# Kernel tuning notes

Measured on AMD Instinct MI355X. Metric: run time of the kernel, lower is better.

The kernel has to match this reference:

```python
import jax, jax.numpy as jnp
import numpy as np

C = 1024
D = C // 8  # query/key channel dim


def setup_inputs() -> dict:
    key = jax.random.key(0)
    ks = jax.random.split(key, 8)
    x = jax.random.normal(ks[0], (8, C, 2048), dtype=jnp.float32)
    # 1x1 Conv1d == per-position linear over channels: weight [out, in], bias [out]
    s_qk = 1.0 / np.sqrt(C)
    Wq = jax.random.uniform(ks[1], (D, C), jnp.float32, -s_qk, s_qk)
    bq = jax.random.uniform(ks[2], (D,), jnp.float32, -s_qk, s_qk)
    Wk = jax.random.uniform(ks[3], (D, C), jnp.float32, -s_qk, s_qk)
    bk = jax.random.uniform(ks[4], (D,), jnp.float32, -s_qk, s_qk)
    Wv = jax.random.uniform(ks[5], (C, C), jnp.float32, -s_qk, s_qk)
    bv = jax.random.uniform(ks[6], (C,), jnp.float32, -s_qk, s_qk)
    gamma = jnp.zeros((1,), dtype=jnp.float32)
    return {"x": x, "Wq": Wq, "bq": bq, "Wk": Wk, "bk": bk, "Wv": Wv, "bv": bv, "gamma": gamma}


def reference(x, Wq, bq, Wk, bk, Wv, bv, gamma):
    # x: [b, c, l]
    q = jnp.einsum('dc,bcl->bdl', Wq, x) + bq[None, :, None]  # [b, d, l]
    k = jnp.einsum('dc,bcl->bdl', Wk, x) + bk[None, :, None]  # [b, d, l]
    v = jnp.einsum('oc,bcl->bol', Wv, x) + bv[None, :, None]  # [b, c, l]
    energy = jnp.einsum('bdi,bdj->bij', q, k)                  # [b, l, l] (no scale, as in source)
    attention = jax.nn.softmax(energy, axis=-1)
    out = jnp.einsum('bcj,bij->bci', v, attention)             # value @ attention^T
    return gamma * out + x
```

## Files before the change

kernel.cpp:

```cpp
#include <hip/hip_runtime.h>
#include <hip/hip_bf16.h>
#include <stdint.h>

#define B_ 8
#define C_ 1024
#define D_ 128
#define L_ 2048

typedef __attribute__((ext_vector_type(8))) short short8;
typedef __attribute__((ext_vector_type(4))) float floatx4;

#define GLDS16(g, l)                                                          \
    __builtin_amdgcn_global_load_lds(                                         \
        (const __attribute__((address_space(1))) uint32_t*)(g),               \
        (__attribute__((address_space(3))) uint32_t*)(l), 16, 0, 0)

__device__ inline float b2f(uint16_t u) {
    union { uint32_t i; float f; } x; x.i = (uint32_t)u << 16; return x.f;
}
__device__ inline uint16_t f2b(float f) {
    union { uint32_t i; float f; } x; x.f = f;
    uint32_t r = (x.i + 0x7fff + ((x.i >> 16) & 1)) >> 16;
    return (uint16_t)r;
}

__global__ void cast_f32_bf16(const float* __restrict__ src, uint16_t* __restrict__ dst, int n) {
    int i = blockIdx.x * 256 + threadIdx.x;
    if (i < n) dst[i] = f2b(src[i]);
}

__global__ __launch_bounds__(256) void transpose_cast(const float* __restrict__ x, uint16_t* __restrict__ xT) {
    __shared__ float tile[32][33];
    int b = blockIdx.z;
    int l0 = blockIdx.x * 32, c0 = blockIdx.y * 32;
    int tx = threadIdx.x, ty = threadIdx.y;
    const float* xb = x + (size_t)b * C_ * L_;
#pragma unroll
    for (int i = 0; i < 4; i++)
        tile[ty + i * 8][tx] = xb[(size_t)(c0 + ty + i * 8) * L_ + l0 + tx];
    __syncthreads();
    uint16_t* xtb = xT + (size_t)b * L_ * C_;
#pragma unroll
    for (int i = 0; i < 4; i++) {
        int l = l0 + ty + i * 8, c = c0 + tx;
        xtb[(size_t)l * C_ + c] = f2b(tile[tx][ty + i * 8]);
    }
}

template <int EPI>
__global__ __launch_bounds__(256) void gemm_nt(
    const uint16_t* __restrict__ A, const uint16_t* __restrict__ B,
    long sA, long sB, const float* __restrict__ bias,
    void* __restrict__ Cout, long sC, int ldc,
    int N, int K, const float* __restrict__ gamma, const float* __restrict__ X) {

    __shared__ uint4 As4[512];
    __shared__ uint4 Bs4[512];
    uint16_t* As = (uint16_t*)As4;
    uint16_t* Bs = (uint16_t*)Bs4;

    const int b = blockIdx.z;
    const uint16_t* Ab = A + (size_t)b * sA;
    const uint16_t* Bb = B + (size_t)b * sB;
    const int m0 = blockIdx.y * 128;
    const int n0 = blockIdx.x * 128;

    const int t = threadIdx.x;
    const int lane = t & 63;
    const int wave = t >> 6;
    const int wm = (wave >> 1) * 64;
    const int wn = (wave & 1) * 64;

    floatx4 acc[4][4] = {};

    const int c0 = t, c1 = t + 256;
    const uint16_t* gA0 = Ab + (size_t)(m0 + (c0 >> 2)) * K + (c0 & 3) * 8;
    const uint16_t* gA1 = Ab + (size_t)(m0 + (c1 >> 2)) * K + (c1 & 3) * 8;
    const uint16_t* gB0 = Bb + (size_t)(n0 + (c0 >> 2)) * K + (c0 & 3) * 8;
    const uint16_t* gB1 = Bb + (size_t)(n0 + (c1 >> 2)) * K + (c1 & 3) * 8;

    for (int k0 = 0; k0 < K; k0 += 32) {
        __syncthreads();
        GLDS16(gA0 + k0, &As4[c0]);
        GLDS16(gA1 + k0, &As4[c1]);
        GLDS16(gB0 + k0, &Bs4[c0]);
        GLDS16(gB1 + k0, &Bs4[c1]);
        __syncthreads();

        const int kg = (lane >> 4) * 8;
        const int rA = wm + (lane & 15);
        const int rB = wn + (lane & 15);
        short8 af[4], bf[4];
#pragma unroll
        for (int i = 0; i < 4; i++) af[i] = *(const short8*)(As + (rA + i * 16) * 32 + kg);
#pragma unroll
        for (int j = 0; j < 4; j++) bf[j] = *(const short8*)(Bs + (rB + j * 16) * 32 + kg);
#pragma unroll
        for (int i = 0; i < 4; i++)
#pragma unroll
            for (int j = 0; j < 4; j++)
                acc[i][j] = __builtin_amdgcn_mfma_f32_16x16x32_bf16(af[i], bf[j], acc[i][j], 0, 0, 0);
    }

    if (EPI == 0 || EPI == 1 || EPI == 2) {
        uint16_t* Cb = (uint16_t*)Cout + (size_t)b * sC;
#pragma unroll
        for (int i = 0; i < 4; i++) {
#pragma unroll
            for (int j = 0; j < 4; j++) {
                int mrow = m0 + wm + i * 16 + ((lane >> 4) << 2);
                int ncol = n0 + wn + j * 16 + (lane & 15);
#pragma unroll
                for (int r = 0; r < 4; r++) {
                    float val = acc[i][j][r];
                    if (EPI == 0 || EPI == 1) val += bias[mrow + r];
                    if (EPI == 1)
                        Cb[(size_t)ncol * ldc + mrow + r] = f2b(val);
                    else
                        Cb[(size_t)(mrow + r) * ldc + ncol] = f2b(val);
                }
            }
        }
    } else {
        float g = gamma[0];
        float* Ob = (float*)Cout + (size_t)b * sC;
        const float* Xb = X + (size_t)b * sC;
#pragma unroll
        for (int i = 0; i < 4; i++) {
#pragma unroll
            for (int j = 0; j < 4; j++) {
                int mrow = m0 + wm + i * 16 + ((lane >> 4) << 2);
                int ncol = n0 + wn + j * 16 + (lane & 15);
#pragma unroll
                for (int r = 0; r < 4; r++) {
                    size_t idx = (size_t)(mrow + r) * ldc + ncol;
                    Ob[idx] = g * acc[i][j][r] + Xb[idx];
                }
            }
        }
    }
}

__global__ __launch_bounds__(256) void softmax_rows(uint16_t* __restrict__ att) {
    const int i = blockIdx.x, b = blockIdx.y;
    uint16_t* row = att + ((size_t)b * L_ + i) * L_;
    const int t = threadIdx.x;
    short8 v = *(const short8*)(row + t * 8);
    float f[8];
    float m = -1e30f;
#pragma unroll
    for (int e = 0; e < 8; e++) { f[e] = b2f((uint16_t)v[e]); m = fmaxf(m, f[e]); }
#pragma unroll
    for (int off = 32; off >= 1; off >>= 1) m = fmaxf(m, __shfl_xor(m, off));
    __shared__ float redm[4], reds[4];
    const int wave = t >> 6;
    if ((t & 63) == 0) redm[wave] = m;
    __syncthreads();
    m = fmaxf(fmaxf(redm[0], redm[1]), fmaxf(redm[2], redm[3]));
    float s = 0.f;
#pragma unroll
    for (int e = 0; e < 8; e++) { f[e] = __expf(f[e] - m); s += f[e]; }
#pragma unroll
    for (int off = 32; off >= 1; off >>= 1) s += __shfl_xor(s, off);
    if ((t & 63) == 0) reds[wave] = s;
    __syncthreads();
    s = reds[0] + reds[1] + reds[2] + reds[3];
    float inv = 1.0f / s;
    short8 o;
#pragma unroll
    for (int e = 0; e < 8; e++) o[e] = (short)f2b(f[e] * inv);
    *(short8*)(row + t * 8) = o;
}

#define OFF_XT   0ull
#define OFF_Q    33554432ull
#define OFF_K    37748736ull
#define OFF_V    41943040ull
#define OFF_ATT  75497472ull
#define OFF_WQ   142606336ull
#define OFF_WK   142868480ull
#define OFF_WV   143130624ull

extern "C" void kernel_launch(void* const* d_in, const int* in_sizes, int n_in,
                              void* d_out, int out_size, void* d_ws, size_t ws_size,
                              hipStream_t stream) {
    const float* x  = (const float*)d_in[0];
    const float* Wq = (const float*)d_in[1];
    const float* bq = (const float*)d_in[2];
    const float* Wk = (const float*)d_in[3];
    const float* bk = (const float*)d_in[4];
    const float* Wv = (const float*)d_in[5];
    const float* bv = (const float*)d_in[6];
    const float* gamma = (const float*)d_in[7];
    float* out = (float*)d_out;
    char* ws = (char*)d_ws;

    uint16_t* xT   = (uint16_t*)(ws + OFF_XT);
    uint16_t* q    = (uint16_t*)(ws + OFF_Q);
    uint16_t* k    = (uint16_t*)(ws + OFF_K);
    uint16_t* v    = (uint16_t*)(ws + OFF_V);
    uint16_t* att  = (uint16_t*)(ws + OFF_ATT);
    uint16_t* Wqb  = (uint16_t*)(ws + OFF_WQ);
    uint16_t* Wkb  = (uint16_t*)(ws + OFF_WK);
    uint16_t* Wvb  = (uint16_t*)(ws + OFF_WV);

    cast_f32_bf16<<<dim3((D_ * C_ + 255) / 256), 256, 0, stream>>>(Wq, Wqb, D_ * C_);
    cast_f32_bf16<<<dim3((D_ * C_ + 255) / 256), 256, 0, stream>>>(Wk, Wkb, D_ * C_);
    cast_f32_bf16<<<dim3((C_ * C_ + 255) / 256), 256, 0, stream>>>(Wv, Wvb, C_ * C_);

    transpose_cast<<<dim3(L_ / 32, C_ / 32, B_), dim3(32, 8), 0, stream>>>(x, xT);

    gemm_nt<1><<<dim3(L_ / 128, 1, B_), 256, 0, stream>>>(
        Wqb, xT, 0, (long)L_ * C_, bq, q, (long)L_ * D_, D_, L_, C_, nullptr, nullptr);
    gemm_nt<1><<<dim3(L_ / 128, 1, B_), 256, 0, stream>>>(
        Wkb, xT, 0, (long)L_ * C_, bk, k, (long)L_ * D_, D_, L_, C_, nullptr, nullptr);
    gemm_nt<0><<<dim3(L_ / 128, C_ / 128, B_), 256, 0, stream>>>(
        Wvb, xT, 0, (long)L_ * C_, bv, v, (long)C_ * L_, L_, L_, C_, nullptr, nullptr);

    gemm_nt<2><<<dim3(L_ / 128, L_ / 128, B_), 256, 0, stream>>>(
        q, k, (long)L_ * D_, (long)L_ * D_, nullptr, att, (long)L_ * L_, L_, L_, D_, nullptr, nullptr);

    softmax_rows<<<dim3(L_, B_), 256, 0, stream>>>(att);

    gemm_nt<3><<<dim3(L_ / 128, C_ / 128, B_), 256, 0, stream>>>(
        v, att, (long)C_ * L_, (long)L_ * L_, nullptr, out, (long)C_ * L_, L_, L_, L_, gamma, x);
}
```

Baseline: 401.3 us.

## Use 256x256 double-buffered GEMM tiles and fuse Q/K projections

After: 355.4 us. -11.5%, faster.

```diff
diff --git a/kernel.cpp b/kernel.cpp
--- a/kernel.cpp
+++ b/kernel.cpp
@@ -47,12 +47,10 @@
     }
 }
 
-template <int EPI>
-__global__ __launch_bounds__(256) void gemm_nt(
-    const uint16_t* __restrict__ A, const uint16_t* __restrict__ B,
-    long sA, long sB, const float* __restrict__ bias,
-    void* __restrict__ Cout, long sC, int ldc,
-    int N, int K, const float* __restrict__ gamma, const float* __restrict__ X) {
+__global__ __launch_bounds__(256) void gemm_qk(
+    const uint16_t* __restrict__ A, const uint16_t* __restrict__ B, long sB,
+    const float* __restrict__ bq, const float* __restrict__ bk,
+    uint16_t* __restrict__ Cout, long sC, int K) {
 
     __shared__ uint4 As4[512];
     __shared__ uint4 Bs4[512];
@@ -60,7 +58,7 @@
     uint16_t* Bs = (uint16_t*)Bs4;
 
     const int b = blockIdx.z;
-    const uint16_t* Ab = A + (size_t)b * sA;
+    const uint16_t* Ab = A;
     const uint16_t* Bb = B + (size_t)b * sB;
     const int m0 = blockIdx.y * 128;
     const int n0 = blockIdx.x * 128;
@@ -102,42 +100,119 @@
                 acc[i][j] = __builtin_amdgcn_mfma_f32_16x16x32_bf16(af[i], bf[j], acc[i][j], 0, 0, 0);
     }
 
-    if (EPI == 0 || EPI == 1 || EPI == 2) {
+    uint16_t* Cb = Cout + (size_t)b * sC;
+#pragma unroll
+    for (int i = 0; i < 4; i++)
+#pragma unroll
+        for (int j = 0; j < 4; j++) {
+            int mrow = m0 + wm + i * 16 + ((lane >> 4) << 2);
+            int ncol = n0 + wn + j * 16 + (lane & 15);
+#pragma unroll
+            for (int r = 0; r < 4; r++) {
+                int mr = mrow + r;
+                float val = acc[i][j][r] + (mr < 128 ? bq[mr] : bk[mr - 128]);
+                Cb[(size_t)ncol * 256 + mr] = f2b(val);
+            }
+        }
+}
+
+template <int EPI>
+__global__ __launch_bounds__(512, 2) void gemm256(
+    const uint16_t* __restrict__ A, const uint16_t* __restrict__ B,
+    int lda, int ldb, long sA, long sB, const float* __restrict__ bias,
+    void* __restrict__ Cout, long sC, int ldc, int K,
+    const float* __restrict__ gamma, const float* __restrict__ X) {
+
+    __shared__ uint4 As4[2][2048];
+    __shared__ uint4 Bs4[2][2048];
+
+    const int b = blockIdx.z;
+    const uint16_t* Ab = A + (size_t)b * sA;
+    const uint16_t* Bb = B + (size_t)b * sB;
+    const int m0 = blockIdx.y * 256;
+    const int n0 = blockIdx.x * 256;
+
+    const int t = threadIdx.x;
+    const int lane = t & 63;
+    const int wid = t >> 6;
+    const int wm = (wid >> 2) * 128;
+    const int wn = (wid & 3) * 64;
+
+    const int srow = t >> 3;
+    const int schunk = (t & 7) * 8;
+    const uint16_t* gA = Ab + (size_t)(m0 + srow) * lda + schunk;
+    const uint16_t* gB = Bb + (size_t)(n0 + srow) * ldb + schunk;
+
+    floatx4 acc[8][4] = {};
+    const int nt = K >> 6;
+
+#define STAGE256(p, k0)                                                      \
+    {                                                                        \
+        _Pragma("unroll") for (int r = 0; r < 4; r++) {                      \
+            GLDS16(gA + (size_t)(64 * r) * lda + (k0), &As4[p][t + 512 * r]);\
+            GLDS16(gB + (size_t)(64 * r) * ldb + (k0), &Bs4[p][t + 512 * r]);\
+        }                                                                    \
+    }
+
+    STAGE256(0, 0);
+    __syncthreads();
+
+    for (int kt = 0; kt < nt; kt++) {
+        const int cur = kt & 1;
+        if (kt + 1 < nt) STAGE256(cur ^ 1, (kt + 1) * 64);
+
+        const uint16_t* Ac = (const uint16_t*)As4[cur];
+        const uint16_t* Bc = (const uint16_t*)Bs4[cur];
+        const int ra = (wm + (lane & 15)) * 64 + (lane >> 4) * 8;
+        const int rb = (wn + (lane & 15)) * 64 + (lane >> 4) * 8;
+#pragma unroll
+        for (int ks = 0; ks < 2; ks++) {
+            short8 af[8], bf[4];
+#pragma unroll
+            for (int mi = 0; mi < 8; mi++) af[mi] = *(const short8*)(Ac + ra + mi * (16 * 64) + ks * 32);
+#pragma unroll
+            for (int nj = 0; nj < 4; nj++) bf[nj] = *(const short8*)(Bc + rb + nj * (16 * 64) + ks * 32);
+#pragma unroll
+            for (int mi = 0; mi < 8; mi++)
+#pragma unroll
+                for (int nj = 0; nj < 4; nj++)
+                    acc[mi][nj] = __builtin_amdgcn_mfma_f32_16x16x32_bf16(af[mi], bf[nj], acc[mi][nj], 0, 0, 0);
+        }
+        __syncthreads();
+    }
+#undef STAGE256
+
+    if (EPI == 0 || EPI == 2) {
         uint16_t* Cb = (uint16_t*)Cout + (size_t)b * sC;
 #pragma unroll
-        for (int i = 0; i < 4; i++) {
-#pragma unroll
-            for (int j = 0; j < 4; j++) {
-                int mrow = m0 + wm + i * 16 + ((lane >> 4) << 2);
-                int ncol = n0 + wn + j * 16 + (lane & 15);
+        for (int mi = 0; mi < 8; mi++)
+#pragma unroll
+            for (int nj = 0; nj < 4; nj++) {
+                int mrow = m0 + wm + mi * 16 + ((lane >> 4) << 2);
+                int ncol = n0 + wn + nj * 16 + (lane & 15);
 #pragma unroll
                 for (int r = 0; r < 4; r++) {
-                    float val = acc[i][j][r];
-                    if (EPI == 0 || EPI == 1) val += bias[mrow + r];
-                    if (EPI == 1)
-                        Cb[(size_t)ncol * ldc + mrow + r] = f2b(val);
-                    else
-                        Cb[(size_t)(mrow + r) * ldc + ncol] = f2b(val);
+                    float val = acc[mi][nj][r];
+                    if (EPI == 0) val += bias[mrow + r];
+                    Cb[(size_t)(mrow + r) * ldc + ncol] = f2b(val);
                 }
             }
-        }
     } else {
         float g = gamma[0];
         float* Ob = (float*)Cout + (size_t)b * sC;
         const float* Xb = X + (size_t)b * sC;
 #pragma unroll
-        for (int i = 0; i < 4; i++) {
-#pragma unroll
-            for (int j = 0; j < 4; j++) {
-                int mrow = m0 + wm + i * 16 + ((lane >> 4) << 2);
-                int ncol = n0 + wn + j * 16 + (lane & 15);
+        for (int mi = 0; mi < 8; mi++)
+#pragma unroll
+            for (int nj = 0; nj < 4; nj++) {
+                int mrow = m0 + wm + mi * 16 + ((lane >> 4) << 2);
+                int ncol = n0 + wn + nj * 16 + (lane & 15);
 #pragma unroll
                 for (int r = 0; r < 4; r++) {
                     size_t idx = (size_t)(mrow + r) * ldc + ncol;
-                    Ob[idx] = g * acc[i][j][r] + Xb[idx];
+                    Ob[idx] = g * acc[mi][nj][r] + Xb[idx];
                 }
             }
-        }
     }
 }
 
@@ -173,12 +248,10 @@
 }
 
 #define OFF_XT   0ull
-#define OFF_Q    33554432ull
-#define OFF_K    37748736ull
+#define OFF_QK   33554432ull
 #define OFF_V    41943040ull
 #define OFF_ATT  75497472ull
-#define OFF_WQ   142606336ull
-#define OFF_WK   142868480ull
+#define OFF_WQK  142606336ull
 #define OFF_WV   143130624ull
 
 extern "C" void kernel_launch(void* const* d_in, const int* in_sizes, int n_in,
@@ -196,32 +269,31 @@
     char* ws = (char*)d_ws;
 
     uint16_t* xT   = (uint16_t*)(ws + OFF_XT);
-    uint16_t* q    = (uint16_t*)(ws + OFF_Q);
-    uint16_t* k    = (uint16_t*)(ws + OFF_K);
+    uint16_t* qk   = (uint16_t*)(ws + OFF_QK);
     uint16_t* v    = (uint16_t*)(ws + OFF_V);
     uint16_t* att  = (uint16_t*)(ws + OFF_ATT);
-    uint16_t* Wqb  = (uint16_t*)(ws + OFF_WQ);
-    uint16_t* Wkb  = (uint16_t*)(ws + OFF_WK);
+    uint16_t* Wqkb = (uint16_t*)(ws + OFF_WQK);
     uint16_t* Wvb  = (uint16_t*)(ws + OFF_WV);
 
-    cast_f32_bf16<<<dim3((D_ * C_ + 255) / 256), 256, 0, stream>>>(Wq, Wqb, D_ * C_);
-    cast_f32_bf16<<<dim3((D_ * C_ + 255) / 256), 256, 0, stream>>>(Wk, Wkb, D_ * C_);
+    cast_f32_bf16<<<dim3((D_ * C_ + 255) / 256), 256, 0, stream>>>(Wq, Wqkb, D_ * C_);
+    cast_f32_bf16<<<dim3((D_ * C_ + 255) / 256), 256, 0, stream>>>(Wk, Wqkb + D_ * C_, D_ * C_);
     cast_f32_bf16<<<dim3((C_ * C_ + 255) / 256), 256, 0, stream>>>(Wv, Wvb, C_ * C_);
 
     transpose_cast<<<dim3(L_ / 32, C_ / 32, B_), dim3(32, 8), 0, stream>>>(x, xT);
 
-    gemm_nt<1><<<dim3(L_ / 128, 1, B_), 256, 0, stream>>>(
-        Wqb, xT, 0, (long)L_ * C_, bq, q, (long)L_ * D_, D_, L_, C_, nullptr, nullptr);
-    gemm_nt<1><<<dim3(L_ / 128, 1, B_), 256, 0, stream>>>(
-        Wkb, xT, 0, (long)L_ * C_, bk, k, (long)L_ * D_, D_, L_, C_, nullptr, nullptr);
-    gemm_nt<0><<<dim3(L_ / 128, C_ / 128, B_), 256, 0, stream>>>(
-        Wvb, xT, 0, (long)L_ * C_, bv, v, (long)C_ * L_, L_, L_, C_, nullptr, nullptr);
-
-    gemm_nt<2><<<dim3(L_ / 128, L_ / 128, B_), 256, 0, stream>>>(
-        q, k, (long)L_ * D_, (long)L_ * D_, nullptr, att, (long)L_ * L_, L_, L_, D_, nullptr, nullptr);
+    gemm_qk<<<dim3(L_ / 128, 2, B_), 256, 0, stream>>>(
+        Wqkb, xT, (long)L_ * C_, bq, bk, qk, (long)L_ * 256, C_);
+
+    gemm256<0><<<dim3(L_ / 256, C_ / 256, B_), 512, 0, stream>>>(
+        Wvb, xT, C_, C_, 0, (long)L_ * C_, bv, v, (long)C_ * L_, L_, C_, nullptr, nullptr);
+
+    gemm256<2><<<dim3(L_ / 256, L_ / 256, B_), 512, 0, stream>>>(
+        qk, qk + 128, 256, 256, (long)L_ * 256, (long)L_ * 256, nullptr,
+        att, (long)L_ * L_, L_, D_, nullptr, nullptr);
 
     softmax_rows<<<dim3(L_, B_), 256, 0, stream>>>(att);
 
-    gemm_nt<3><<<dim3(L_ / 128, C_ / 128, B_), 256, 0, stream>>>(
-        v, att, (long)C_ * L_, (long)L_ * L_, nullptr, out, (long)C_ * L_, L_, L_, L_, gamma, x);
-}
+    gemm256<3><<<dim3(L_ / 256, C_ / 256, B_), 512, 0, stream>>>(
+        v, att, L_, L_, (long)C_ * L_, (long)L_ * L_, nullptr,
+        out, (long)C_ * L_, L_, L_, gamma, x);
+}
```
